# Kernel tuning notes

Hardware: AMD Instinct MI355X
Metric: run time of the kernel (lower is better)

Reference implementation:

```python
import jax, jax.numpy as jnp
from jax import lax
import numpy as np

B, T, UMAX, D = 32, 128, 64, 512
U1 = UMAX + 1
BLANK = D - 1  # blank=-1 -> last vocab slot
NEG = -1e30    # finite -inf surrogate (keeps logaddexp grads NaN-free)


def setup_inputs() -> dict:
    key = jax.random.key(0)
    k1, k2, k3, k4 = jax.random.split(key, 4)
    logits = jax.random.normal(k1, (B, T, U1, D), dtype=jnp.float32)
    logit_lengths = jax.random.randint(k2, (B,), T // 2, T + 1, dtype=jnp.int32)
    target_lengths = jax.random.randint(k3, (B,), UMAX // 2, UMAX + 1, dtype=jnp.int32)
    targets = jax.random.randint(k4, (B, UMAX), 0, D - 1, dtype=jnp.int32)  # never blank
    return {"logits": logits, "logit_lengths": logit_lengths,
            "target_lengths": target_lengths, "targets": targets}


def _transducer_costs(log_probs, logit_lengths, target_lengths, targets):
    """RNN-T alpha DP; costs[b] = -(alpha[T_b-1, U_b] + lp_blank[T_b-1, U_b])."""
    b, t_max, u1, d = log_probs.shape
    lp_blank = log_probs[..., BLANK]                                   # [B,T,U1]
    tgt_pad = jnp.concatenate([targets, jnp.zeros((b, 1), targets.dtype)], axis=1)  # [B,U1]
    lp_emit = jnp.take_along_axis(log_probs, tgt_pad[:, None, :, None], axis=3)[..., 0]  # [B,T,U1]
    u_idx = jnp.arange(u1)
    # emit transitions only exist for u < target_length (masks padded labels too)
    lp_emit = jnp.where(u_idx[None, None, :] < target_lengths[:, None, None], lp_emit, NEG)

    # alpha[0, u] = cumsum of emit log-probs along u
    row0 = jnp.concatenate(
        [jnp.zeros((b, 1), jnp.float32), jnp.cumsum(lp_emit[:, 0, :-1], axis=1)], axis=1)

    def row_step(prev_row, xs):
        lpb_prev, lpe = xs                      # both [B,U1]
        skip = prev_row + lpb_prev              # alpha[t-1,u] + blank(t-1,u)

        def inner(a_left, xu):
            s_u, e_um1 = xu                      # skip[:,u], lp_emit[:,t,u-1]
            a = jnp.logaddexp(s_u, a_left + e_um1)
            return a, a

        a0 = skip[:, 0]
        _, rest = lax.scan(inner, a0,
                           (jnp.moveaxis(skip[:, 1:], 1, 0),
                            jnp.moveaxis(lpe[:, :-1], 1, 0)))
        row = jnp.concatenate([a0[:, None], jnp.moveaxis(rest, 0, 1)], axis=1)
        return row, row

    xs = (jnp.moveaxis(lp_blank[:, :-1, :], 1, 0),   # blank at row t-1
          jnp.moveaxis(lp_emit[:, 1:, :], 1, 0))     # emit at row t
    _, rows = lax.scan(row_step, row0, xs)
    alpha = jnp.concatenate([row0[:, None, :], jnp.moveaxis(rows, 0, 1)], axis=1)  # [B,T,U1]

    bi = jnp.arange(b)
    tf = logit_lengths - 1
    uf = target_lengths
    return -(alpha[bi, tf, uf] + lp_blank[bi, tf, uf])


def reference(logits, logit_lengths, target_lengths, targets):
    lp = jax.nn.log_softmax(logits, axis=-1)
    return _transducer_costs(lp, logit_lengths, target_lengths, targets)
```

## Files before the change

kernel.cpp:

```cpp
#include <hip/hip_runtime.h>

#define BQ 32
#define TQ 128
#define U1Q 65
#define UMAXQ 64
#define DQ 512
#define SLAB (TQ * U1Q)
#define PSTRIDE 66
#define PSLAB (TQ * PSTRIDE)
#define NCELLS (BQ * SLAB)
#define NEGQ (-1e30f)
#define L2E 1.4426950408889634f
#define LN2F 0.6931471805599453f

typedef float f4 __attribute__((ext_vector_type(4)));

#define EXP2(x) __builtin_amdgcn_exp2f(x)
#define LOG2(x) __builtin_amdgcn_logf(x)

__device__ __forceinline__ float logadd2(float x, float y) {
    float mx = fmaxf(x, y);
    float d  = fminf(x, y) - mx;
    return mx + LOG2(1.0f + EXP2(d));
}

__global__ __launch_bounds__(512) void lse_k(const float* __restrict__ logits,
                                             const int* __restrict__ targets,
                                             const int* __restrict__ llen,
                                             const int* __restrict__ tlen,
                                             float* __restrict__ ws) {
    int wid  = (blockIdx.x * 512 + threadIdx.x) >> 6;
    int lane = threadIdx.x & 63;
    int h = lane >> 3;
    int i = lane & 7;
    int r = wid * 8 + h;

    int b = r / SLAB;
    int q = r - b * SLAB;
    int t = q / U1Q;
    int u = q - t * U1Q;
    int tl = tlen[b];
    if (t >= llen[b] || u > tl) return;

    const f4* rp = (const f4*)(logits + (size_t)r * DQ) + i;
    f4 w0 = rp[0],   w1 = rp[8],   w2 = rp[16],  w3 = rp[24],
       w4 = rp[32],  w5 = rp[40],  w6 = rp[48],  w7 = rp[56],
       w8 = rp[64],  w9 = rp[72],  wA = rp[80],  wB = rp[88],
       wC = rp[96],  wD = rp[104], wE = rp[112], wF = rp[120];

#define SUM4(v) (EXP2((v).x * L2E) + EXP2((v).y * L2E) + \
                 EXP2((v).z * L2E) + EXP2((v).w * L2E))
    float s0 = (SUM4(w0) + SUM4(w1)) + (SUM4(w2) + SUM4(w3));
    float s1 = (SUM4(w4) + SUM4(w5)) + (SUM4(w6) + SUM4(w7));
    float s2 = (SUM4(w8) + SUM4(w9)) + (SUM4(wA) + SUM4(wB));
    float s3 = (SUM4(wC) + SUM4(wD)) + (SUM4(wE) + SUM4(wF));
    float s = (s0 + s1) + (s2 + s3);
#pragma unroll
    for (int d = 1; d <= 4; d <<= 1) s += __shfl_xor(s, d, 64);

    float l2s = LOG2(s);
    float* wb = ws + (size_t)b * 2 * SLAB;

    if (i == 7) wb[q] = fmaf(wF.w, L2E, -l2s);

    int tgt = targets[b * UMAXQ + (u < UMAXQ ? u : UMAXQ - 1)];
    int itgt = (tgt >> 2) & 7;
    if (i == itgt) {
        int ktgt = tgt >> 5, jt = tgt & 3;
        f4 c = w0;
        if (ktgt == 1)  c = w1;
        if (ktgt == 2)  c = w2;
        if (ktgt == 3)  c = w3;
        if (ktgt == 4)  c = w4;
        if (ktgt == 5)  c = w5;
        if (ktgt == 6)  c = w6;
        if (ktgt == 7)  c = w7;
        if (ktgt == 8)  c = w8;
        if (ktgt == 9)  c = w9;
        if (ktgt == 10) c = wA;
        if (ktgt == 11) c = wB;
        if (ktgt == 12) c = wC;
        if (ktgt == 13) c = wD;
        if (ktgt == 14) c = wE;
        if (ktgt == 15) c = wF;
        float val = (jt == 0) ? c.x : ((jt == 1) ? c.y : ((jt == 2) ? c.z : c.w));
        wb[SLAB + q] = (u < tl) ? fmaf(val, L2E, -l2s) : NEGQ;
    }
}

__global__ __launch_bounds__(512) void dp_k(const float* __restrict__ ws,
                                            const int* __restrict__ llen,
                                            const int* __restrict__ tlen,
                                            float* __restrict__ out) {
    __shared__ float S[2 * PSLAB];
    int b   = blockIdx.x;
    int tid = threadIdx.x;

    int tf = llen[b] - 1;
    int uf = tlen[b];

    const f4* srcB = (const f4*)(ws + (size_t)b * 2 * SLAB);
    const f4* srcE = srcB + SLAB / 4;
    float* SBp = S;
    float* SEp = S + PSLAB;
    int nelem = (tf + 1) * U1Q;
    int nb4 = (nelem + 3) >> 2;
    for (int idx = tid; idx < nb4; idx += 512) {
        f4 vb = srcB[idx];
        f4 ve = srcE[idx];
        int e0 = idx * 4;
#pragma unroll
        for (int j = 0; j < 4; ++j) {
            int e = e0 + j;
            if (e < nelem) {
                int t = e / 65;
                int p = t * PSTRIDE + (e - t * 65);
                SBp[p] = vb[j];
                SEp[p] = ve[j];
            }
        }
    }
    __syncthreads();
    if (tid >= 64) return;

    int lane = tid;
    const float* SB = SBp;
    const float* SE = SEp;

    int kmax = tf + uf;

    float a   = (lane == 0) ? 0.0f : NEGQ;
    float a64 = NEGQ;
    int um1 = (lane > 0) ? lane - 1 : 0;

    auto LB = [&](int k) { int t = k - lane - 1; t = t < 0 ? 0 : (t > TQ - 1 ? TQ - 1 : t);
                           return SB[t * PSTRIDE + lane]; };
    auto LE = [&](int k) { int t = k - lane;     t = t < 0 ? 0 : (t > TQ - 1 ? TQ - 1 : t);
                           return SE[t * PSTRIDE + um1]; };
    auto LB6 = [&](int k) { int t = k - 65; t = t < 0 ? 0 : (t > TQ - 1 ? TQ - 1 : t);
                            return SB[t * PSTRIDE + 64]; };
    auto LE6 = [&](int k) { int t = k - 64; t = t < 0 ? 0 : (t > TQ - 1 ? TQ - 1 : t);
                            return SE[t * PSTRIDE + 63]; };

#define STEP(kk, lbv, lev, lb6v, le6v) do {                                  \
    int k_ = (kk); int t = k_ - lane;                                        \
    float A   = (t >= 1) ? (a + (lbv)) : NEGQ;                               \
    float ash = __shfl_up(a, 1, 64);                                         \
    float Bv  = (lane >= 1 && t >= 0) ? (ash + (lev)) : NEGQ;                \
    float a63 = __shfl(a, 63, 64);                                           \
    float anew = logadd2(A, Bv);                                             \
    int t64 = k_ - 64;                                                       \
    float A64 = (t64 >= 1) ? (a64 + (lb6v)) : NEGQ;                          \
    float B64 = (t64 >= 0) ? (a63 + (le6v)) : NEGQ;                          \
    a64 = (t64 >= 0) ? logadd2(A64, B64) : NEGQ;                             \
    a = anew;                                                                \
} while (0)

    float lbA = LB(1), leA = LE(1), lb6A = LB6(1), le6A = LE6(1);
    float lbB = LB(2), leB = LE(2), lb6B = LB6(2), le6B = LE6(2);
    float lbC = LB(3), leC = LE(3), lb6C = LB6(3), le6C = LE6(3);
    float lbD = LB(4), leD = LE(4), lb6D = LB6(4), le6D = LE6(4);

    int k = 1;
    for (; k + 3 <= kmax; k += 4) {
        STEP(k,     lbA, leA, lb6A, le6A); lbA = LB(k + 4); leA = LE(k + 4); lb6A = LB6(k + 4); le6A = LE6(k + 4);
        STEP(k + 1, lbB, leB, lb6B, le6B); lbB = LB(k + 5); leB = LE(k + 5); lb6B = LB6(k + 5); le6B = LE6(k + 5);
        STEP(k + 2, lbC, leC, lb6C, le6C); lbC = LB(k + 6); leC = LE(k + 6); lb6C = LB6(k + 6); le6C = LE6(k + 6);
        STEP(k + 3, lbD, leD, lb6D, le6D); lbD = LB(k + 7); leD = LE(k + 7); lb6D = LB6(k + 7); le6D = LE6(k + 7);
    }
    if (k <= kmax) { STEP(k, lbA, leA, lb6A, le6A); k++; }
    if (k <= kmax) { STEP(k, lbB, leB, lb6B, le6B); k++; }
    if (k <= kmax) { STEP(k, lbC, leC, lb6C, le6C); k++; }

    float alpha_f = (uf >= 64) ? a64 : __shfl(a, uf, 64);
    if (lane == 0) out[b] = -(alpha_f + SB[tf * PSTRIDE + uf]) * LN2F;
}

extern "C" void kernel_launch(void* const* d_in, const int* in_sizes, int n_in,
                              void* d_out, int out_size, void* d_ws, size_t ws_size,
                              hipStream_t stream) {
    const float* logits  = (const float*)d_in[0];
    const int*   llen    = (const int*)d_in[1];
    const int*   tlen    = (const int*)d_in[2];
    const int*   targets = (const int*)d_in[3];
    float*       out     = (float*)d_out;
    float*       ws      = (float*)d_ws;

    int blocks = NCELLS / 64;
    lse_k<<<blocks, 512, 0, stream>>>(logits, targets, llen, tlen, ws);
    dp_k<<<BQ, 512, 0, stream>>>(ws, llen, tlen, out);
}
```

Before: 78.41 us.

## Restructure LSE kernel so each wave loads eight contiguous rows coalesced

The log-softmax kernel now has each wave read a contiguous block of 8 rows, with every lane reading 16-byte chunks at stride 64, so the whole 16 KB span is loaded in fully coalesced accesses. Before, each 8-lane group handled one row at strided offsets. The per-row reductions now run a full 64-lane xor shuffle across 8 independent sums, which costs more shuffle instructions. Dead rows are masked per row, but a wave still loads all 8 rows if any one of them is alive, so memory traffic on partially dead groups may go up.

```diff
diff --git a/kernel.cpp b/kernel.cpp
--- a/kernel.cpp
+++ b/kernel.cpp
@@ -29,62 +29,62 @@
                                              const int* __restrict__ llen,
                                              const int* __restrict__ tlen,
                                              float* __restrict__ ws) {
-    int wid  = (blockIdx.x * 512 + threadIdx.x) >> 6;
-    int lane = threadIdx.x & 63;
-    int h = lane >> 3;
-    int i = lane & 7;
-    int r = wid * 8 + h;
+    int tid = threadIdx.x;
+    int w = tid >> 6, l = tid & 63;
+    int r0 = (blockIdx.x * 8 + w) * 8;
+    int b  = r0 / SLAB;
+    int q0 = r0 - b * SLAB;
+    int tl = tlen[b];
+    int ll = llen[b];
 
-    int b = r / SLAB;
-    int q = r - b * SLAB;
-    int t = q / U1Q;
-    int u = q - t * U1Q;
-    int tl = tlen[b];
-    if (t >= llen[b] || u > tl) return;
+    int  uA[8]; bool alive[8]; bool any = false;
+#pragma unroll
+    for (int p = 0; p < 8; ++p) {
+        int q = q0 + p;
+        int t = q / U1Q;
+        int u = q - t * U1Q;
+        uA[p] = u;
+        alive[p] = (t < ll) && (u <= tl);
+        any |= alive[p];
+    }
+    if (!any) return;
 
-    const f4* rp = (const f4*)(logits + (size_t)r * DQ) + i;
-    f4 w0 = rp[0],   w1 = rp[8],   w2 = rp[16],  w3 = rp[24],
-       w4 = rp[32],  w5 = rp[40],  w6 = rp[48],  w7 = rp[56],
-       w8 = rp[64],  w9 = rp[72],  wA = rp[80],  wB = rp[88],
-       wC = rp[96],  wD = rp[104], wE = rp[112], wF = rp[120];
+    const f4* bp = (const f4*)(logits + (size_t)r0 * DQ);
+    f4 wv[16];
+#pragma unroll
+    for (int j = 0; j < 16; ++j) wv[j] = bp[j * 64 + l];
 
 #define SUM4(v) (EXP2((v).x * L2E) + EXP2((v).y * L2E) + \
                  EXP2((v).z * L2E) + EXP2((v).w * L2E))
-    float s0 = (SUM4(w0) + SUM4(w1)) + (SUM4(w2) + SUM4(w3));
-    float s1 = (SUM4(w4) + SUM4(w5)) + (SUM4(w6) + SUM4(w7));
-    float s2 = (SUM4(w8) + SUM4(w9)) + (SUM4(wA) + SUM4(wB));
-    float s3 = (SUM4(wC) + SUM4(wD)) + (SUM4(wE) + SUM4(wF));
-    float s = (s0 + s1) + (s2 + s3);
+    float s[8];
 #pragma unroll
-    for (int d = 1; d <= 4; d <<= 1) s += __shfl_xor(s, d, 64);
+    for (int p = 0; p < 8; ++p)
+        s[p] = alive[p] ? (SUM4(wv[2 * p]) + SUM4(wv[2 * p + 1])) : 1.0f;
 
-    float l2s = LOG2(s);
+#pragma unroll
+    for (int d = 1; d < 64; d <<= 1) {
+#pragma unroll
+        for (int p = 0; p < 8; ++p)
+            if (alive[p]) s[p] += __shfl_xor(s[p], d, 64);
+    }
+
     float* wb = ws + (size_t)b * 2 * SLAB;
-
-    if (i == 7) wb[q] = fmaf(wF.w, L2E, -l2s);
-
-    int tgt = targets[b * UMAXQ + (u < UMAXQ ? u : UMAXQ - 1)];
-    int itgt = (tgt >> 2) & 7;
-    if (i == itgt) {
-        int ktgt = tgt >> 5, jt = tgt & 3;
-        f4 c = w0;
-        if (ktgt == 1)  c = w1;
-        if (ktgt == 2)  c = w2;
-        if (ktgt == 3)  c = w3;
-        if (ktgt == 4)  c = w4;
-        if (ktgt == 5)  c = w5;
-        if (ktgt == 6)  c = w6;
-        if (ktgt == 7)  c = w7;
-        if (ktgt == 8)  c = w8;
-        if (ktgt == 9)  c = w9;
-        if (ktgt == 10) c = wA;
-        if (ktgt == 11) c = wB;
-        if (ktgt == 12) c = wC;
-        if (ktgt == 13) c = wD;
-        if (ktgt == 14) c = wE;
-        if (ktgt == 15) c = wF;
-        float val = (jt == 0) ? c.x : ((jt == 1) ? c.y : ((jt == 2) ? c.z : c.w));
-        wb[SLAB + q] = (u < tl) ? fmaf(val, L2E, -l2s) : NEGQ;
+#pragma unroll
+    for (int p = 0; p < 8; ++p) {
+        if (!alive[p]) continue;
+        float l2s = LOG2(s[p]);
+        int q = q0 + p;
+        if (l == 63) wb[q] = fmaf(wv[2 * p + 1].w, L2E, -l2s);
+        int u = uA[p];
+        int tg = targets[b * UMAXQ + (u < UMAXQ ? u : UMAXQ - 1)];
+        if (l == ((tg >> 2) & 63)) {
+            int j = tg & 3;
+            f4 c0 = wv[2 * p], c1 = wv[2 * p + 1];
+            float e0 = (j == 0) ? c0.x : ((j == 1) ? c0.y : ((j == 2) ? c0.z : c0.w));
+            float e1 = (j == 0) ? c1.x : ((j == 1) ? c1.y : ((j == 2) ? c1.z : c1.w));
+            float val = (tg & 256) ? e1 : e0;
+            wb[SLAB + q] = (u < tl) ? fmaf(val, L2E, -l2s) : NEGQ;
+        }
     }
 }
 
```

Result: slower. 109.1 us (+39.1%).
